# Kernel optimization log

Measured on AMD Instinct MI355X. Metric: run time of the kernel, lower is better.

The kernel has to match this reference:

```python
import jax, jax.numpy as jnp
import numpy as np

NCE_T = 0.07   # opt.nce_T
EPS = 1e-8     # torch CosineSimilarity eps
DIAG_FILL = -10.0

N, D = 8192, 256

def setup_inputs() -> dict:
    key = jax.random.key(0)
    kq, kk = jax.random.split(key)
    feat_q = jax.random.normal(kq, (N, D), dtype=jnp.float32)
    feat_k = jax.random.normal(kk, (N, D), dtype=jnp.float32)
    return {"feat_q": feat_q, "feat_k": feat_k}

def reference(feat_q, feat_k):
    # feat_k is detached in the original
    feat_k = jax.lax.stop_gradient(feat_k)
    nq = jnp.linalg.norm(feat_q, axis=-1)            # [N]
    nk = jnp.linalg.norm(feat_k, axis=-1)            # [N]
    # positive cosine similarity (paired rows)
    l_pos = jnp.sum(feat_q * feat_k, axis=-1) / jnp.maximum(nq * nk, EPS)  # [N]
    # full N x N cosine similarity via GEMM (torch does a broadcasted version)
    sim = (feat_q @ feat_k.T) / jnp.maximum(nq[:, None] * nk[None, :], EPS)  # [N,N]
    # mask self-similarities with -10.0 BEFORE dividing by temperature
    diag = jnp.eye(sim.shape[0], dtype=bool)
    l_neg = jnp.where(diag, DIAG_FILL, sim)
    out = jnp.concatenate([l_pos[:, None], l_neg], axis=1) / NCE_T  # [N, N+1]
    # cross-entropy vs target class 0, reduction='none'
    loss = jax.scipy.special.logsumexp(out, axis=1) - out[:, 0]     # [N]
    return loss
```

## Files before the change

### kernel.cpp

```cpp
#include <hip/hip_runtime.h>
#include <stdint.h>
#include <math.h>

#define NROWS 8192
#define DDIM  256
#define BM    128
#define BN    128
#define GJ    8
#define COLS_PER_GROUP (NROWS / GJ)

constexpr float INV_T  = 1.0f / 0.07f;
constexpr float LOG2E  = 1.44269504f;
constexpr float K1     = INV_T * LOG2E;

typedef __bf16 bf16x8 __attribute__((ext_vector_type(8)));
typedef float  f32x4  __attribute__((ext_vector_type(4)));

__device__ __forceinline__ void async_copy16(const uint16_t* g, uint16_t* l) {
    __builtin_amdgcn_global_load_lds(
        (const __attribute__((address_space(1))) uint32_t*)g,
        (__attribute__((address_space(3))) uint32_t*)l, 16, 0, 0);
}

__device__ inline uint16_t f2bf(float f) {
    uint32_t u = __float_as_uint(f);
    u += 0x7fffu + ((u >> 16) & 1u);
    return (uint16_t)(u >> 16);
}

__global__ __launch_bounds__(256) void norm_convert_kernel(
    const float* __restrict__ fq, const float* __restrict__ fk,
    uint16_t* __restrict__ qb, uint16_t* __restrict__ kb)
{
    const int wave = threadIdx.x >> 6;
    const int lane = threadIdx.x & 63;
    const int row  = blockIdx.x * 4 + wave;

    const float* src; uint16_t* dstb;
    if (row < NROWS) {
        src = fq + (size_t)row * DDIM; dstb = qb + (size_t)row * DDIM;
    } else {
        int r = row - NROWS;
        src = fk + (size_t)r * DDIM; dstb = kb + (size_t)r * DDIM;
    }

    float4 v = ((const float4*)src)[lane];
    float ss = v.x*v.x + v.y*v.y + v.z*v.z + v.w*v.w;
    #pragma unroll
    for (int m = 1; m < 64; m <<= 1) ss += __shfl_xor(ss, m, 64);
    float r = rsqrtf(ss);

    ushort4 o;
    o.x = f2bf(v.x * r); o.y = f2bf(v.y * r); o.z = f2bf(v.z * r); o.w = f2bf(v.w * r);
    ((ushort4*)dstb)[lane] = o;
}

__global__ __launch_bounds__(256, 2) void nce_main_kernel(
    const uint16_t* __restrict__ qb, const uint16_t* __restrict__ kb,
    float* __restrict__ lpT, float* __restrict__ gpl)
{
    __shared__ __align__(16) uint16_t lds_k[4 * BN * 32];

    const int tid    = threadIdx.x;
    const int wave   = tid >> 6;
    const int lane   = tid & 63;
    const int quad   = lane >> 4;
    const int lanelo = lane & 15;
    const int wr     = wave >> 1;
    const int wc     = wave & 1;
    const int rowBase      = blockIdx.x * BM;
    const int colGroupBase = blockIdx.y * COLS_PER_GROUP;

    bf16x8 aq[4][8];
    #pragma unroll
    for (int mt = 0; mt < 4; ++mt) {
        const uint16_t* qrow =
            qb + (size_t)(rowBase + wr * 64 + mt * 16 + lanelo) * DDIM + quad * 8;
        #pragma unroll
        for (int kk = 0; kk < 8; ++kk)
            aq[mt][kk] = *(const bf16x8*)(qrow + kk * 32);
    }

    int kS0   = wave * 128 + lane;
    int krow0 = kS0 >> 2;
    int kch0  = (lane & 3) ^ (krow0 & 3);
    int krow1 = (kS0 + 64) >> 2;
    int kch1  = (lane & 3) ^ (krow1 & 3);
    const uint16_t* kbase0 = kb + (size_t)(colGroupBase + krow0) * DDIM + kch0 * 8;
    const uint16_t* kbase1 = kb + (size_t)(colGroupBase + krow1) * DDIM + kch1 * 8;

    #pragma unroll
    for (int p = 0; p < 3; ++p) {
        uint16_t* ld = lds_k + (p << 12) + (wave << 10);
        async_copy16(kbase0 + (p << 5), ld);
        async_copy16(kbase1 + (p << 5), ld + 512);
    }

    int bvoff[4];
    #pragma unroll
    for (int nt = 0; nt < 4; ++nt) {
        int rk = wc * 64 + nt * 16 + lanelo;
        bvoff[nt] = rk * 32 + (quad ^ (rk & 3)) * 8;
    }

    float l_run[16];
    #pragma unroll
    for (int i = 0; i < 16; ++i) l_run[i] = 0.f;

    for (int jt = 0; jt < 8; ++jt) {
        const int colT = colGroupBase + jt * BN;

        f32x4 acc[4][4];
        #pragma unroll
        for (int mt = 0; mt < 4; ++mt)
            #pragma unroll
            for (int nt = 0; nt < 4; ++nt)
                acc[mt][nt] = (f32x4){0.f, 0.f, 0.f, 0.f};

        #pragma unroll
        for (int kk = 0; kk < 8; ++kk) {
            const int p = (jt << 3) + kk;

            asm volatile("s_waitcnt vmcnt(4)" ::: "memory");
            __builtin_amdgcn_s_barrier();

            {
                const int np  = p + 3;
                const int npm = np & 63;
                const int off = ((npm >> 3) << 15) + ((npm & 7) << 5);
                uint16_t* ld = lds_k + ((np & 3) << 12) + (wave << 10);
                async_copy16(kbase0 + off, ld);
                async_copy16(kbase1 + off, ld + 512);
            }

            bf16x8 bv[4];
            const int bufo = (p & 3) << 12;
            #pragma unroll
            for (int nt = 0; nt < 4; ++nt)
                bv[nt] = *(const bf16x8*)&lds_k[bufo + bvoff[nt]];

            __builtin_amdgcn_s_setprio(1);
            #pragma unroll
            for (int mt = 0; mt < 4; ++mt)
                #pragma unroll
                for (int nt = 0; nt < 4; ++nt)
                    acc[mt][nt] = __builtin_amdgcn_mfma_f32_16x16x32_bf16(
                        aq[mt][kk], bv[nt], acc[mt][nt], 0, 0, 0);
            __builtin_amdgcn_s_setprio(0);
        }

        int gcol[4];
        #pragma unroll
        for (int nt = 0; nt < 4; ++nt) gcol[nt] = colT + wc * 64 + nt * 16 + lanelo;
        #pragma unroll
        for (int mt = 0; mt < 4; ++mt) {
            #pragma unroll
            for (int rg = 0; rg < 4; ++rg) {
                int grow = rowBase + wr * 64 + mt * 16 + quad * 4 + rg;
                float s = 0.f;
                #pragma unroll
                for (int nt = 0; nt < 4; ++nt) {
                    float a = acc[mt][nt][rg];
                    float e = exp2f(fmaf(a, K1, -K1));
                    if (grow == gcol[nt]) { lpT[grow] = a * INV_T; e = 0.f; }
                    s += e;
                }
                l_run[mt * 4 + rg] += s;
            }
        }
    }

    #pragma unroll
    for (int i = 0; i < 16; ++i) {
        float v = l_run[i];
        v += __shfl_xor(v, 1, 64);
        v += __shfl_xor(v, 2, 64);
        v += __shfl_xor(v, 4, 64);
        v += __shfl_xor(v, 8, 64);
        l_run[i] = v;
    }

    __syncthreads();

    float* pl = (float*)lds_k;
    if (lanelo == 0) {
        #pragma unroll
        for (int mt = 0; mt < 4; ++mt)
            #pragma unroll
            for (int rg = 0; rg < 4; ++rg) {
                int lr = wr * 64 + mt * 16 + quad * 4 + rg;
                pl[wc * 128 + lr] = l_run[mt * 4 + rg];
            }
    }
    __syncthreads();
    if (tid < 128) {
        float L = pl[tid] + pl[128 + tid];
        gpl[(size_t)blockIdx.y * NROWS + rowBase + tid] = L;
    }
}

__global__ __launch_bounds__(256) void finalize_kernel(
    const float* __restrict__ gpl, const float* __restrict__ lpT,
    float* __restrict__ out)
{
    int t = blockIdx.x * 256 + threadIdx.x;
    if (t >= NROWS) return;
    float L = 0.f;
    #pragma unroll
    for (int g = 0; g < GJ; ++g) L += gpl[g * NROWS + t];
    float lp = lpT[t];
    L += __expf(lp - INV_T);
    out[t] = INV_T + __logf(L) - lp;
}

extern "C" void kernel_launch(void* const* d_in, const int* in_sizes, int n_in,
                              void* d_out, int out_size, void* d_ws, size_t ws_size,
                              hipStream_t stream) {
    const float* fq = (const float*)d_in[0];
    const float* fk = (const float*)d_in[1];
    char* ws = (char*)d_ws;
    uint16_t* qb  = (uint16_t*)(ws);
    uint16_t* kb  = (uint16_t*)(ws + 4194304);
    float*    lpT = (float*)(ws + 8388608);
    float*    gpl = (float*)(ws + 8421376);

    norm_convert_kernel<<<(2 * NROWS) / 4, 256, 0, stream>>>(fq, fk, qb, kb);
    dim3 grid(NROWS / BM, GJ);
    nce_main_kernel<<<grid, 256, 0, stream>>>(qb, kb, lpT, gpl);
    finalize_kernel<<<NROWS / 256, 256, 0, stream>>>(gpl, lpT, (float*)d_out);
}
```

Baseline: 116.5 us.

## Split main kernel across eight waves with two row tiles each

Moves the main GEMM+exp kernel from 256 to 512 threads per block. Each wave now owns 32 rows instead of 64, which halves the Q register fragments and accumulators per thread, and each wave issues one async K copy per stage instead of two. The LDS swizzle is changed to XOR on row>>2 to match the new load mapping. The aim is more waves in flight to hide latency, at the cost of each B fragment read from LDS being reused by fewer MFMAs and more barrier participants.

```diff
diff --git a/kernel.cpp b/kernel.cpp
--- a/kernel.cpp
+++ b/kernel.cpp
@@ -55,7 +55,7 @@
     ((ushort4*)dstb)[lane] = o;
 }
 
-__global__ __launch_bounds__(256, 2) void nce_main_kernel(
+__global__ __launch_bounds__(512, 2) void nce_main_kernel(
     const uint16_t* __restrict__ qb, const uint16_t* __restrict__ kb,
     float* __restrict__ lpT, float* __restrict__ gpl)
 {
@@ -71,48 +71,42 @@
     const int rowBase      = blockIdx.x * BM;
     const int colGroupBase = blockIdx.y * COLS_PER_GROUP;
 
-    bf16x8 aq[4][8];
-    #pragma unroll
-    for (int mt = 0; mt < 4; ++mt) {
+    bf16x8 aq[2][8];
+    #pragma unroll
+    for (int mt = 0; mt < 2; ++mt) {
         const uint16_t* qrow =
-            qb + (size_t)(rowBase + wr * 64 + mt * 16 + lanelo) * DDIM + quad * 8;
+            qb + (size_t)(rowBase + wr * 32 + mt * 16 + lanelo) * DDIM + quad * 8;
         #pragma unroll
         for (int kk = 0; kk < 8; ++kk)
             aq[mt][kk] = *(const bf16x8*)(qrow + kk * 32);
     }
 
-    int kS0   = wave * 128 + lane;
-    int krow0 = kS0 >> 2;
-    int kch0  = (lane & 3) ^ (krow0 & 3);
-    int krow1 = (kS0 + 64) >> 2;
-    int kch1  = (lane & 3) ^ (krow1 & 3);
-    const uint16_t* kbase0 = kb + (size_t)(colGroupBase + krow0) * DDIM + kch0 * 8;
-    const uint16_t* kbase1 = kb + (size_t)(colGroupBase + krow1) * DDIM + kch1 * 8;
-
-    #pragma unroll
-    for (int p = 0; p < 3; ++p) {
-        uint16_t* ld = lds_k + (p << 12) + (wave << 10);
-        async_copy16(kbase0 + (p << 5), ld);
-        async_copy16(kbase1 + (p << 5), ld + 512);
-    }
+    const int kS   = wave * 64 + lane;
+    const int krow = kS >> 2;
+    const int kch  = (lane & 3) ^ ((krow >> 2) & 3);
+    const uint16_t* kbase = kb + (size_t)(colGroupBase + krow) * DDIM + kch * 8;
+
+    #pragma unroll
+    for (int p = 0; p < 3; ++p)
+        async_copy16(kbase + (p << 5), lds_k + (p << 12) + (wave << 9));
 
     int bvoff[4];
     #pragma unroll
     for (int nt = 0; nt < 4; ++nt) {
         int rk = wc * 64 + nt * 16 + lanelo;
-        bvoff[nt] = rk * 32 + (quad ^ (rk & 3)) * 8;
-    }
-
-    float l_run[16];
-    #pragma unroll
-    for (int i = 0; i < 16; ++i) l_run[i] = 0.f;
+        bvoff[nt] = rk * 32 + (quad ^ (lanelo >> 2)) * 8;
+    }
+
+    float l_run[8];
+    #pragma unroll
+    for (int i = 0; i < 8; ++i) l_run[i] = 0.f;
 
     for (int jt = 0; jt < 8; ++jt) {
         const int colT = colGroupBase + jt * BN;
 
-        f32x4 acc[4][4];
-        #pragma unroll
-        for (int mt = 0; mt < 4; ++mt)
+        f32x4 acc[2][4];
+        #pragma unroll
+        for (int mt = 0; mt < 2; ++mt)
             #pragma unroll
             for (int nt = 0; nt < 4; ++nt)
                 acc[mt][nt] = (f32x4){0.f, 0.f, 0.f, 0.f};
@@ -121,16 +115,14 @@
         for (int kk = 0; kk < 8; ++kk) {
             const int p = (jt << 3) + kk;
 
-            asm volatile("s_waitcnt vmcnt(4)" ::: "memory");
-            __builtin_amdgcn_s_barrier();
+            asm volatile("s_waitcnt vmcnt(2)" ::: "memory");
+            asm volatile("s_barrier" ::: "memory");
 
             {
-                const int np  = p + 3;
-                const int npm = np & 63;
+                const int npm = (p + 3) & 63;
                 const int off = ((npm >> 3) << 15) + ((npm & 7) << 5);
-                uint16_t* ld = lds_k + ((np & 3) << 12) + (wave << 10);
-                async_copy16(kbase0 + off, ld);
-                async_copy16(kbase1 + off, ld + 512);
+                async_copy16(kbase + off,
+                             lds_k + (((p + 3) & 3) << 12) + (wave << 9));
             }
 
             bf16x8 bv[4];
@@ -141,7 +133,7 @@
 
             __builtin_amdgcn_s_setprio(1);
             #pragma unroll
-            for (int mt = 0; mt < 4; ++mt)
+            for (int mt = 0; mt < 2; ++mt)
                 #pragma unroll
                 for (int nt = 0; nt < 4; ++nt)
                     acc[mt][nt] = __builtin_amdgcn_mfma_f32_16x16x32_bf16(
@@ -153,10 +145,10 @@
         #pragma unroll
         for (int nt = 0; nt < 4; ++nt) gcol[nt] = colT + wc * 64 + nt * 16 + lanelo;
         #pragma unroll
-        for (int mt = 0; mt < 4; ++mt) {
+        for (int mt = 0; mt < 2; ++mt) {
             #pragma unroll
             for (int rg = 0; rg < 4; ++rg) {
-                int grow = rowBase + wr * 64 + mt * 16 + quad * 4 + rg;
+                int grow = rowBase + wr * 32 + mt * 16 + quad * 4 + rg;
                 float s = 0.f;
                 #pragma unroll
                 for (int nt = 0; nt < 4; ++nt) {
@@ -171,7 +163,7 @@
     }
 
     #pragma unroll
-    for (int i = 0; i < 16; ++i) {
+    for (int i = 0; i < 8; ++i) {
         float v = l_run[i];
         v += __shfl_xor(v, 1, 64);
         v += __shfl_xor(v, 2, 64);
@@ -185,10 +177,10 @@
     float* pl = (float*)lds_k;
     if (lanelo == 0) {
         #pragma unroll
-        for (int mt = 0; mt < 4; ++mt)
+        for (int mt = 0; mt < 2; ++mt)
             #pragma unroll
             for (int rg = 0; rg < 4; ++rg) {
-                int lr = wr * 64 + mt * 16 + quad * 4 + rg;
+                int lr = wr * 32 + mt * 16 + quad * 4 + rg;
                 pl[wc * 128 + lr] = l_run[mt * 4 + rg];
             }
     }
@@ -226,6 +218,6 @@
 
     norm_convert_kernel<<<(2 * NROWS) / 4, 256, 0, stream>>>(fq, fk, qb, kb);
     dim3 grid(NROWS / BM, GJ);
-    nce_main_kernel<<<grid, 256, 0, stream>>>(qb, kb, lpT, gpl);
+    nce_main_kernel<<<grid, 512, 0, stream>>>(qb, kb, lpT, gpl);
     finalize_kernel<<<NROWS / 256, 256, 0, stream>>>(gpl, lpT, (float*)d_out);
 }
```

New measurement: 121.7 us. +4.5%, slower.
